# Kernel optimization log

Measured on AMD Instinct MI355X. Metric: run time of the kernel, lower is better.

Reference implementation:

```python
import jax, jax.numpy as jnp
import numpy as np
import math

D, H, FF = 1024, 16, 4096
B, L = 4, 1024

def setup_inputs() -> dict:
    key = jax.random.key(0)
    ks = jax.random.split(key, 20)
    g = lambda k, shp: jax.random.normal(k, shp, dtype=jnp.float32) * 0.02
    inp = {
        'x': jax.random.normal(ks[0], (B, L, D), dtype=jnp.float32),
        'encoder_output': jax.random.normal(ks[1], (B, L, D), dtype=jnp.float32),
        'src_mask': jnp.ones((1, 1, L, L), dtype=jnp.int32),
        'tgt_mask': jnp.tril(jnp.ones((L, L), dtype=jnp.int32))[None, None],
        'wq': g(ks[2], (D, D)), 'bq': jnp.zeros((D,), jnp.float32),
        'wk': g(ks[3], (D, D)), 'bk': jnp.zeros((D,), jnp.float32),
        'wv': g(ks[4], (D, D)), 'bv': jnp.zeros((D,), jnp.float32),
        'wo': g(ks[5], (D, D)), 'bo': jnp.zeros((D,), jnp.float32),
        'w1': g(ks[6], (FF, D)), 'b1': jnp.zeros((FF,), jnp.float32),
        'w2': g(ks[7], (D, FF)), 'b2': jnp.zeros((D,), jnp.float32),
        'g1': jnp.ones((D,), jnp.float32), 'be1': jnp.zeros((D,), jnp.float32),
        'g2': jnp.ones((D,), jnp.float32), 'be2': jnp.zeros((D,), jnp.float32),
    }
    return inp

def _layernorm(x, g, b, eps=1e-5):
    mu = jnp.mean(x, axis=-1, keepdims=True)
    var = jnp.var(x, axis=-1, keepdims=True)
    return (x - mu) * jax.lax.rsqrt(var + eps) * g + b

def _mha(q, k, v, mask, wq, bq, wk, bk, wv, bv, wo, bo):
    Bq, Lq, C = q.shape
    dh = C // H
    qh = (q @ wq.T + bq).reshape(Bq, Lq, H, dh)      # b q h d
    kh = (k @ wk.T + bk).reshape(Bq, -1, H, dh)       # b k h d
    vh = (v @ wv.T + bv).reshape(Bq, -1, H, dh)
    # NOTE: source scales by sqrt(C) (full model dim), not sqrt(head_dim)
    scores = jnp.einsum('bqhd,bkhd->bhqk', qh, kh) / math.sqrt(C)
    if mask is not None:
        scores = jnp.where(mask == 0, jnp.float32(-1e9), scores)
    attn = jax.nn.softmax(scores, axis=-1)
    out = jnp.einsum('bhqk,bkhd->bqhd', attn, vh).reshape(Bq, Lq, C)
    return out @ wo.T + bo

def reference(x, encoder_output, src_mask, tgt_mask,
              wq, bq, wk, bk, wv, bv, wo, bo,
              w1, b1, w2, b2, g1, be1, g2, be2):
    # self-attention (dropout identity in eval mode)
    y1 = _mha(x, x, x, tgt_mask, wq, bq, wk, bk, wv, bv, wo, bo)
    y1 = _layernorm(y1 + x, g1, be1)
    # cross-attention: source reuses attn1 weights and layer_norm1 (faithful)
    y2 = _mha(y1, encoder_output, encoder_output, src_mask, wq, bq, wk, bk, wv, bv, wo, bo)
    y2 = _layernorm(y1 + y2, g1, be1)
    # FFN + layer_norm2
    y = jax.nn.relu(y2 @ w1.T + b1) @ w2.T + b2
    return _layernorm(y2 + y, g2, be2)
```

## Files before the change

### kernel.cpp

```cpp
#include <hip/hip_runtime.h>
#include <hip/hip_bf16.h>

typedef __attribute__((ext_vector_type(8))) short short8;
typedef __attribute__((ext_vector_type(4))) float f32x4;
typedef __attribute__((ext_vector_type(4))) unsigned short ushort4v;

#define MFMA_BF16(a, b, c) __builtin_amdgcn_mfma_f32_16x16x32_bf16((a), (b), (c), 0, 0, 0)
#define AS1 __attribute__((address_space(1)))
#define AS3 __attribute__((address_space(3)))

__device__ __forceinline__ unsigned short f2b(float f) {
  unsigned u = __float_as_uint(f);
  u += 0x7fffu + ((u >> 16) & 1u);
  return (unsigned short)(u >> 16);
}

__device__ __forceinline__ size_t kpack_idx(int row, int col) {
  int b = row >> 10, l = row & 1023, h = col >> 6, d = col & 63;
  return ((size_t)(b * 16 + h) << 16) + l * 64 + (d ^ ((l & 7) << 3));
}

__global__ __launch_bounds__(256) void cast8(
    const float* s0, const float* s1, const float* s2, const float* s3,
    const float* s4, const float* s5, const float* s6, const float* s7,
    unsigned short* d0, unsigned short* d1, unsigned short* d2, unsigned short* d3,
    unsigned short* d4, unsigned short* d5, unsigned short* d6, unsigned short* d7,
    int n0, int n1, int n2, int n3, int n4, int n5, int n6, int n7) {
  const float* s; unsigned short* d; int n;
  switch (blockIdx.y) {
    case 0: s = s0; d = d0; n = n0; break;
    case 1: s = s1; d = d1; n = n1; break;
    case 2: s = s2; d = d2; n = n2; break;
    case 3: s = s3; d = d3; n = n3; break;
    case 4: s = s4; d = d4; n = n4; break;
    case 5: s = s5; d = d5; n = n5; break;
    case 6: s = s6; d = d6; n = n6; break;
    default: s = s7; d = d7; n = n7; break;
  }
  int stride = gridDim.x * blockDim.x;
  for (int i = blockIdx.x * blockDim.x + threadIdx.x; i < n; i += stride) {
    float4 v = reinterpret_cast<const float4*>(s)[i];
    ushort4v o;
    o.x = f2b(v.x); o.y = f2b(v.y); o.z = f2b(v.z); o.w = f2b(v.w);
    reinterpret_cast<ushort4v*>(d)[i] = o;
  }
}

template <int RELU, int RES, int OUTF, int OUTB, int TM>
__global__ __launch_bounds__(256, 4) void gemm_bt(
    const unsigned short* __restrict__ A, const unsigned short* __restrict__ W,
    const float* __restrict__ bias, const float* __restrict__ resid,
    float* __restrict__ outF, unsigned short* __restrict__ outB,
    int M, int N, int K) {
  constexpr int MI = TM / 32;
  __shared__ unsigned short lA[2][TM * 32];
  __shared__ unsigned short lB[2][128 * 32];
  int nbn = N >> 7;
  int nwg = gridDim.x;
  int id = blockIdx.x;
  { int q = nwg >> 3; id = (id & 7) * q + (id >> 3); }
  int m0 = (id / nbn) * TM, n0 = (id % nbn) << 7;
  int lane = threadIdx.x & 63, wave = threadIdx.x >> 6;
  int wr = (wave >> 1) * (TM / 2), wc = (wave & 1) * 64;
  int rq = lane & 15, kq = (lane >> 4) * 8;
  f32x4 acc[MI][4] = {};

  int e0 = threadIdx.x * 8;
#define STAGE_BT(KT, BUF)                                                       \
  {                                                                             \
    _Pragma("unroll") for (int i = 0; i < TM / 64; ++i) {                       \
      int e = e0 + i * 2048;                                                    \
      int row = e >> 5, col = e & 31;                                           \
      __builtin_amdgcn_global_load_lds(                                         \
          (const AS1 void*)(A + (size_t)(m0 + row) * K + (KT) + col),           \
          (AS3 void*)(&lA[BUF][e]), 16, 0, 0);                                  \
    }                                                                           \
    _Pragma("unroll") for (int i = 0; i < 2; ++i) {                             \
      int e = e0 + i * 2048;                                                    \
      int row = e >> 5, col = e & 31;                                           \
      __builtin_amdgcn_global_load_lds(                                         \
          (const AS1 void*)(W + (size_t)(n0 + row) * K + (KT) + col),           \
          (AS3 void*)(&lB[BUF][e]), 16, 0, 0);                                  \
    }                                                                           \
  }

  STAGE_BT(0, 0);
  __syncthreads();
  int nk = K >> 5;
  for (int t = 0; t < nk; ++t) {
    int cur = t & 1;
    if (t + 1 < nk) STAGE_BT((t + 1) << 5, cur ^ 1);
    short8 af[MI], bf[4];
#pragma unroll
    for (int i = 0; i < MI; ++i)
      af[i] = *reinterpret_cast<const short8*>(&lA[cur][(wr + i * 16 + rq) * 32 + kq]);
#pragma unroll
    for (int j = 0; j < 4; ++j)
      bf[j] = *reinterpret_cast<const short8*>(&lB[cur][(wc + j * 16 + rq) * 32 + kq]);
#pragma unroll
    for (int i = 0; i < MI; ++i)
#pragma unroll
      for (int j = 0; j < 4; ++j)
        acc[i][j] = MFMA_BF16(af[i], bf[j], acc[i][j]);
    __syncthreads();
  }
#undef STAGE_BT

  int r0 = (lane >> 4) * 4;
#pragma unroll
  for (int i = 0; i < MI; ++i) {
#pragma unroll
    for (int j = 0; j < 4; ++j) {
      int row = m0 + wr + i * 16 + r0;
      int col = n0 + wc + j * 16 + rq;
      float bv = bias[col];
#pragma unroll
      for (int r = 0; r < 4; ++r) {
        float v = acc[i][j][r] + bv;
        if (RES) v += resid[(size_t)(row + r) * N + col];
        if (RELU) v = fmaxf(v, 0.0f);
        if (OUTF) outF[(size_t)(row + r) * N + col] = v;
        if (OUTB) outB[(size_t)(row + r) * N + col] = f2b(v);
      }
    }
  }
}

__global__ __launch_bounds__(256, 4) void gemm_qkv(
    const unsigned short* __restrict__ xb, const unsigned short* __restrict__ encb,
    const unsigned short* __restrict__ wq, const unsigned short* __restrict__ wk,
    const unsigned short* __restrict__ wv,
    const float* __restrict__ bq, const float* __restrict__ bk, const float* __restrict__ bv,
    unsigned short* __restrict__ qb, unsigned short* __restrict__ kp1,
    unsigned short* __restrict__ vp1, unsigned short* __restrict__ kp2,
    unsigned short* __restrict__ vp2) {
  __shared__ unsigned short lA[2][128 * 32];
  __shared__ unsigned short lB[2][128 * 32];
  int id = blockIdx.x;
  id = (id & 7) * 160 + (id >> 3);
  int im = id / 40, jn = id % 40;
  int sel = jn >> 3;
  int m0 = im << 7, col0 = (jn & 7) << 7;
  const unsigned short* A = (sel < 3) ? xb : encb;
  const unsigned short* Wm = (sel == 0) ? wq : ((sel == 1 || sel == 3) ? wk : wv);
  const float* bias = (sel == 0) ? bq : ((sel == 1 || sel == 3) ? bk : bv);
  int lane = threadIdx.x & 63, wave = threadIdx.x >> 6;
  int wr = (wave >> 1) * 64, wc = (wave & 1) * 64;
  int rq = lane & 15, kq = (lane >> 4) * 8;
  f32x4 acc[4][4] = {};

  int e0 = threadIdx.x * 8;
#define STAGE_QKV(KT, BUF)                                                      \
  {                                                                             \
    _Pragma("unroll") for (int i = 0; i < 2; ++i) {                             \
      int e = e0 + i * 2048;                                                    \
      int row = e >> 5, col = e & 31;                                           \
      __builtin_amdgcn_global_load_lds(                                         \
          (const AS1 void*)(A + (size_t)(m0 + row) * 1024 + (KT) + col),        \
          (AS3 void*)(&lA[BUF][e]), 16, 0, 0);                                  \
      __builtin_amdgcn_global_load_lds(                                         \
          (const AS1 void*)(Wm + (size_t)(col0 + row) * 1024 + (KT) + col),     \
          (AS3 void*)(&lB[BUF][e]), 16, 0, 0);                                  \
    }                                                                           \
  }

  STAGE_QKV(0, 0);
  __syncthreads();
  for (int t = 0; t < 32; ++t) {
    int cur = t & 1;
    if (t + 1 < 32) STAGE_QKV((t + 1) << 5, cur ^ 1);
    short8 af[4], bf[4];
#pragma unroll
    for (int i = 0; i < 4; ++i)
      af[i] = *reinterpret_cast<const short8*>(&lA[cur][(wr + i * 16 + rq) * 32 + kq]);
#pragma unroll
    for (int j = 0; j < 4; ++j)
      bf[j] = *reinterpret_cast<const short8*>(&lB[cur][(wc + j * 16 + rq) * 32 + kq]);
#pragma unroll
    for (int i = 0; i < 4; ++i)
#pragma unroll
      for (int j = 0; j < 4; ++j)
        acc[i][j] = MFMA_BF16(af[i], bf[j], acc[i][j]);
    __syncthreads();
  }
#undef STAGE_QKV

  unsigned short* outp = (sel == 0) ? qb : (sel == 1) ? kp1 : (sel == 2) ? vp1
                         : (sel == 3) ? kp2 : vp2;
  int pack = (sel == 0) ? 0 : ((sel == 1 || sel == 3) ? 1 : 2);
  int r0 = (lane >> 4) * 4;
#pragma unroll
  for (int i = 0; i < 4; ++i) {
#pragma unroll
    for (int j = 0; j < 4; ++j) {
      int row0 = m0 + wr + i * 16 + r0;
      int col = col0 + wc + j * 16 + rq;
      float bv = bias[col];
      if (pack == 2) {
        int b = row0 >> 10, k0 = row0 & 1023, h = col >> 6, d = col & 63;
        size_t idx = ((size_t)((b * 16 + h) * 16 + (k0 >> 6)) << 12) + d * 64 + ((k0 & 63) ^ ((d & 7) << 3));
        ushort4v o;
        o.x = f2b(acc[i][j][0] + bv);
        o.y = f2b(acc[i][j][1] + bv);
        o.z = f2b(acc[i][j][2] + bv);
        o.w = f2b(acc[i][j][3] + bv);
        *reinterpret_cast<ushort4v*>(&outp[idx]) = o;
      } else {
#pragma unroll
        for (int r = 0; r < 4; ++r) {
          int row = row0 + r;
          float v = acc[i][j][r] + bv;
          if (pack == 0) outp[(size_t)row * 1024 + col] = f2b(v);
          else outp[kpack_idx(row, col)] = f2b(v);
        }
      }
    }
  }
}

__device__ __forceinline__ void attn_step(
    const unsigned short* __restrict__ kcur, const unsigned short* __restrict__ vcur,
    unsigned short* __restrict__ plw, const short8* qf,
    f32x4* accd, float& m2, float& lsum,
    int rq, int hi, int kq, int xr, int wave, bool domask) {
  const float SC = 0.04508422f;
  f32x4 st[4];
  __builtin_amdgcn_s_setprio(1);
#pragma unroll
  for (int sub = 0; sub < 4; ++sub) {
    f32x4 z = {0.f, 0.f, 0.f, 0.f};
#pragma unroll
    for (int c = 0; c < 2; ++c) {
      short8 kf = *reinterpret_cast<const short8*>(
          &kcur[(sub * 16 + rq) * 64 + ((c * 32 + hi * 8) ^ xr)]);
      z = MFMA_BF16(kf, qf[c], z);
    }
    st[sub] = z * SC;
  }
  __builtin_amdgcn_s_setprio(0);
  if (domask) {
#pragma unroll
    for (int sub = 0; sub < 4; ++sub)
#pragma unroll
      for (int r = 0; r < 4; ++r)
        if (sub * 16 + hi * 4 + r > wave * 16 + rq) st[sub][r] = -1e9f;
  }
  f32x4 t0 = {fmaxf(st[0][0], st[1][0]), fmaxf(st[0][1], st[1][1]),
              fmaxf(st[0][2], st[1][2]), fmaxf(st[0][3], st[1][3])};
  f32x4 t1 = {fmaxf(st[2][0], st[3][0]), fmaxf(st[2][1], st[3][1]),
              fmaxf(st[2][2], st[3][2]), fmaxf(st[2][3], st[3][3])};
  float mx = fmaxf(fmaxf(fmaxf(t0[0], t1[0]), fmaxf(t0[1], t1[1])),
                   fmaxf(fmaxf(t0[2], t1[2]), fmaxf(t0[3], t1[3])));
  mx = fmaxf(mx, __shfl_xor(mx, 16, 64));
  mx = fmaxf(mx, __shfl_xor(mx, 32, 64));
  float mn = fmaxf(m2, mx);
  float al = exp2f(m2 - mn);
  m2 = mn;
  f32x4 e[4];
#pragma unroll
  for (int sub = 0; sub < 4; ++sub)
#pragma unroll
    for (int r = 0; r < 4; ++r) e[sub][r] = exp2f(st[sub][r] - mn);
  f32x4 s01 = e[0] + e[1], s23 = e[2] + e[3];
  f32x4 s = s01 + s23;
  float ps = (s[0] + s[1]) + (s[2] + s[3]);
  ps += __shfl_xor(ps, 16, 64);
  ps += __shfl_xor(ps, 32, 64);
  lsum = lsum * al + ps;
#pragma unroll
  for (int sub = 0; sub < 4; ++sub) {
    unsigned w0 = (unsigned)f2b(e[sub][0]) | ((unsigned)f2b(e[sub][1]) << 16);
    unsigned w1 = (unsigned)f2b(e[sub][2]) | ((unsigned)f2b(e[sub][3]) << 16);
    uint2 w = make_uint2(w0, w1);
    *reinterpret_cast<uint2*>(&plw[rq * 64 + ((sub * 16 + hi * 4) ^ xr)]) = w;
  }
  float alb[4];
#pragma unroll
  for (int r = 0; r < 4; ++r) alb[r] = __shfl(al, hi * 4 + r, 64);
#pragma unroll
  for (int d = 0; d < 4; ++d)
#pragma unroll
    for (int r = 0; r < 4; ++r) accd[d][r] *= alb[r];
  short8 pf[2];
#pragma unroll
  for (int c = 0; c < 2; ++c)
    pf[c] = *reinterpret_cast<const short8*>(&plw[rq * 64 + ((c * 32 + hi * 8) ^ xr)]);
  __builtin_amdgcn_s_setprio(1);
#pragma unroll
  for (int d = 0; d < 4; ++d) {
#pragma unroll
    for (int c = 0; c < 2; ++c) {
      short8 vf = *reinterpret_cast<const short8*>(
          &vcur[(d * 16 + rq) * 64 + ((c * 32 + hi * 8) ^ xr)]);
      accd[d] = MFMA_BF16(pf[c], vf, accd[d]);
    }
  }
  __builtin_amdgcn_s_setprio(0);
}

__global__ __launch_bounds__(256) void attn_kernel(
    const unsigned short* __restrict__ Q, const unsigned short* __restrict__ Kp,
    const unsigned short* __restrict__ Vp, unsigned short* __restrict__ O, int causal) {
  __shared__ unsigned short kls[2][4096];
  __shared__ unsigned short vls[2][4096];
  __shared__ unsigned short pls[4][1024];
  int id = blockIdx.x;
  int xcd = id & 7, j = id >> 3;
  int bh = xcd * 8 + (j & 7);
  int b = bh >> 4, h = bh & 15;
  int lane = threadIdx.x & 63, wave = threadIdx.x >> 6;
  int rq = lane & 15, hi = lane >> 4, kq = hi * 8;
  int xr = (rq & 7) << 3;
  int sb = wave * 1024 + lane * 8;
  const unsigned short* Kbh = Kp + ((size_t)bh << 16);
  const unsigned short* Vbh = Vp + ((size_t)bh << 16);
  unsigned short* plw = pls[wave];

  int p = j >> 3;
  int qtA = p;
  int qtB = causal ? (15 - p) : (p + 8);
  int lastA = causal ? qtA : 15;
  int nkt = causal ? (qtB + 1) : 16;

  int qrowA = qtA * 64 + wave * 16, qrowB = qtB * 64 + wave * 16;
  short8 qfA[2], qfB[2];
#pragma unroll
  for (int c = 0; c < 2; ++c) {
    qfA[c] = *reinterpret_cast<const short8*>(
        Q + (size_t)(b * 1024 + qrowA + rq) * 1024 + h * 64 + c * 32 + kq);
    qfB[c] = *reinterpret_cast<const short8*>(
        Q + (size_t)(b * 1024 + qrowB + rq) * 1024 + h * 64 + c * 32 + kq);
  }

  float mA = -1e30f, lsA = 0.f, mB = -1e30f, lsB = 0.f;
  f32x4 accA[4] = {}, accB[4] = {};

#pragma unroll
  for (int i = 0; i < 2; ++i) {
    __builtin_amdgcn_global_load_lds((const AS1 void*)(Kbh + sb + i * 512),
                                     (AS3 void*)(&kls[0][sb + i * 512]), 16, 0, 0);
    __builtin_amdgcn_global_load_lds((const AS1 void*)(Vbh + sb + i * 512),
                                     (AS3 void*)(&vls[0][sb + i * 512]), 16, 0, 0);
  }
  __syncthreads();

  int cur = 0;
  for (int kt = 0; kt < nkt; ++kt) {
    if (kt + 1 < nkt) {
      const unsigned short* kg = Kbh + (kt + 1) * 4096 + sb;
      const unsigned short* vg = Vbh + (kt + 1) * 4096 + sb;
#pragma unroll
      for (int i = 0; i < 2; ++i) {
        __builtin_amdgcn_global_load_lds((const AS1 void*)(kg + i * 512),
                                         (AS3 void*)(&kls[cur ^ 1][sb + i * 512]), 16, 0, 0);
        __builtin_amdgcn_global_load_lds((const AS1 void*)(vg + i * 512),
                                         (AS3 void*)(&vls[cur ^ 1][sb + i * 512]), 16, 0, 0);
      }
    }
    attn_step(kls[cur], vls[cur], plw, qfB, accB, mB, lsB, rq, hi, kq, xr, wave,
              causal && kt == qtB);
    if (kt <= lastA)
      attn_step(kls[cur], vls[cur], plw, qfA, accA, mA, lsA, rq, hi, kq, xr, wave,
                causal && kt == qtA);
    __syncthreads();
    cur ^= 1;
  }

  float lbA[4], lbB[4];
#pragma unroll
  for (int r = 0; r < 4; ++r) {
    lbA[r] = 1.0f / __shfl(lsA, hi * 4 + r, 64);
    lbB[r] = 1.0f / __shfl(lsB, hi * 4 + r, 64);
  }
#pragma unroll
  for (int d = 0; d < 4; ++d)
#pragma unroll
    for (int r = 0; r < 4; ++r) {
      O[(size_t)(b * 1024 + qrowA + hi * 4 + r) * 1024 + h * 64 + d * 16 + rq] =
          f2b(accA[d][r] * lbA[r]);
      O[(size_t)(b * 1024 + qrowB + hi * 4 + r) * 1024 + h * 64 + d * 16 + rq] =
          f2b(accB[d][r] * lbB[r]);
    }
}

template <int OUTF, int OUTB>
__global__ __launch_bounds__(256) void ln_kernel(const float* __restrict__ X,
                                                 const float* __restrict__ g,
                                                 const float* __restrict__ be,
                                                 float* __restrict__ outF,
                                                 unsigned short* __restrict__ outB) {
  __shared__ float red[2][4];
  int row = blockIdx.x;
  int t = threadIdx.x;
  const float* xr = X + (size_t)row * 1024;
  float4 v = reinterpret_cast<const float4*>(xr)[t];
  float s = v.x + v.y + v.z + v.w;
  float ss = v.x * v.x + v.y * v.y + v.z * v.z + v.w * v.w;
#pragma unroll
  for (int off = 1; off < 64; off <<= 1) {
    s += __shfl_xor(s, off, 64);
    ss += __shfl_xor(ss, off, 64);
  }
  int wave = t >> 6;
  if ((t & 63) == 0) { red[0][wave] = s; red[1][wave] = ss; }
  __syncthreads();
  s = red[0][0] + red[0][1] + red[0][2] + red[0][3];
  ss = red[1][0] + red[1][1] + red[1][2] + red[1][3];
  float mu = s * (1.f / 1024.f);
  float var = ss * (1.f / 1024.f) - mu * mu;
  float rs = rsqrtf(var + 1e-5f);
  float4 gv = reinterpret_cast<const float4*>(g)[t];
  float4 bv = reinterpret_cast<const float4*>(be)[t];
  float o0 = (v.x - mu) * rs * gv.x + bv.x;
  float o1 = (v.y - mu) * rs * gv.y + bv.y;
  float o2 = (v.z - mu) * rs * gv.z + bv.z;
  float o3 = (v.w - mu) * rs * gv.w + bv.w;
  if (OUTF) {
    float4 o = make_float4(o0, o1, o2, o3);
    reinterpret_cast<float4*>(outF + (size_t)row * 1024)[t] = o;
  }
  if (OUTB) {
    ushort4v o;
    o.x = f2b(o0); o.y = f2b(o1); o.z = f2b(o2); o.w = f2b(o3);
    reinterpret_cast<ushort4v*>(outB + (size_t)row * 1024)[t] = o;
  }
}

extern "C" void kernel_launch(void* const* d_in, const int* in_sizes, int n_in,
                              void* d_out, int out_size, void* d_ws, size_t ws_size,
                              hipStream_t stream) {
  const float* x   = (const float*)d_in[0];
  const float* enc = (const float*)d_in[1];
  const float* wq = (const float*)d_in[4];  const float* bq = (const float*)d_in[5];
  const float* wk = (const float*)d_in[6];  const float* bk = (const float*)d_in[7];
  const float* wv = (const float*)d_in[8];  const float* bv = (const float*)d_in[9];
  const float* wo = (const float*)d_in[10]; const float* bo = (const float*)d_in[11];
  const float* w1 = (const float*)d_in[12]; const float* b1 = (const float*)d_in[13];
  const float* w2 = (const float*)d_in[14]; const float* b2 = (const float*)d_in[15];
  const float* g1 = (const float*)d_in[16]; const float* be1 = (const float*)d_in[17];
  const float* g2 = (const float*)d_in[18]; const float* be2 = (const float*)d_in[19];
  float* out = (float*)d_out;

  const int M = 4096;
  char* ws = (char*)d_ws;
  size_t off = 0;
  auto alloc = [&](size_t bytes) -> char* {
    char* p = ws + off;
    off += (bytes + 255) & ~(size_t)255;
    return p;
  };
  unsigned short* xb   = (unsigned short*)alloc((size_t)M * 1024 * 2);
  unsigned short* encb = (unsigned short*)alloc((size_t)M * 1024 * 2);
  unsigned short* wqb  = (unsigned short*)alloc((size_t)1024 * 1024 * 2);
  unsigned short* wkb  = (unsigned short*)alloc((size_t)1024 * 1024 * 2);
  unsigned short* wvb  = (unsigned short*)alloc((size_t)1024 * 1024 * 2);
  unsigned short* wob  = (unsigned short*)alloc((size_t)1024 * 1024 * 2);
  unsigned short* w1b  = (unsigned short*)alloc((size_t)4096 * 1024 * 2);
  unsigned short* w2b  = (unsigned short*)alloc((size_t)4096 * 1024 * 2);
  unsigned short* qb   = (unsigned short*)alloc((size_t)M * 1024 * 2);
  unsigned short* kp1  = (unsigned short*)alloc((size_t)M * 1024 * 2);
  unsigned short* vp1  = (unsigned short*)alloc((size_t)M * 1024 * 2);
  unsigned short* kp2  = (unsigned short*)alloc((size_t)M * 1024 * 2);
  unsigned short* vp2  = (unsigned short*)alloc((size_t)M * 1024 * 2);
  unsigned short* ab   = (unsigned short*)alloc((size_t)M * 1024 * 2);
  float* s1 = (float*)alloc((size_t)M * 1024 * 4);
  float* y1 = (float*)alloc((size_t)M * 1024 * 4);
  unsigned short* hb = kp1;
  unsigned short* y1b = xb;
  unsigned short* y2b = qb;
  float* y2 = y1;

  dim3 b256(256);
  cast8<<<dim3(256, 8), b256, 0, stream>>>(
      x, enc, wq, wk, wv, wo, w1, w2,
      xb, encb, wqb, wkb, wvb, wob, w1b, w2b,
      M * 1024 / 4, M * 1024 / 4, 262144, 262144, 262144, 262144,
      4096 * 1024 / 4, 4096 * 1024 / 4);

  gemm_qkv<<<1280, b256, 0, stream>>>(xb, encb, wqb, wkb, wvb, bq, bk, bv,
                                      qb, kp1, vp1, kp2, vp2);

  attn_kernel<<<512, b256, 0, stream>>>(qb, kp1, vp1, ab, 1);
  gemm_bt<0, 1, 1, 0, 64><<<512, b256, 0, stream>>>(ab, wob, bo, x, s1, nullptr, M, 1024, 1024);
  ln_kernel<1, 1><<<4096, b256, 0, stream>>>(s1, g1, be1, y1, y1b);

  gemm_bt<0, 0, 0, 1, 64><<<512, b256, 0, stream>>>(y1b, wqb, bq, nullptr, nullptr, qb, M, 1024, 1024);
  attn_kernel<<<512, b256, 0, stream>>>(qb, kp2, vp2, ab, 0);
  gemm_bt<0, 1, 1, 0, 64><<<512, b256, 0, stream>>>(ab, wob, bo, y1, s1, nullptr, M, 1024, 1024);
  ln_kernel<1, 1><<<4096, b256, 0, stream>>>(s1, g1, be1, y2, y2b);

  gemm_bt<1, 0, 0, 1, 128><<<1024, b256, 0, stream>>>(y2b, w1b, b1, nullptr, nullptr, hb, M, 4096, 1024);
  gemm_bt<0, 1, 1, 0, 64><<<512, b256, 0, stream>>>(hb, w2b, b2, y2, s1, nullptr, M, 1024, 4096);
  ln_kernel<1, 0><<<4096, b256, 0, stream>>>(s1, g2, be2, out, nullptr);

  (void)in_sizes; (void)n_in; (void)out_size; (void)ws_size;
}
```

Measured before the change: 362.3 us.

## Triple-buffer GEMM LDS staging with vmcnt waits and single barrier per k-step

Converts the double-buffered global-to-LDS staging in the generic and QKV GEMMs to a three-stage ring buffer that prefetches two k-tiles ahead. Each iteration waits only on the oldest loads with an explicit partial vmcnt and uses a single barrier instead of two. This hides more global-load latency behind MFMA work. The cost is 50% more LDS per block, which may reduce occupancy at launch_bounds(256,4), and the wait counts must exactly match the number of issued loads.

```diff
diff --git a/kernel.cpp b/kernel.cpp
--- a/kernel.cpp
+++ b/kernel.cpp
@@ -18,6 +18,15 @@
 __device__ __forceinline__ size_t kpack_idx(int row, int col) {
   int b = row >> 10, l = row & 1023, h = col >> 6, d = col & 63;
   return ((size_t)(b * 16 + h) << 16) + l * 64 + (d ^ ((l & 7) << 3));
+}
+
+template <int N>
+__device__ __forceinline__ void wait_vm() {
+  if constexpr (N == 0) asm volatile("s_waitcnt vmcnt(0)" ::: "memory");
+  else if constexpr (N == 3) asm volatile("s_waitcnt vmcnt(3)" ::: "memory");
+  else if constexpr (N == 4) asm volatile("s_waitcnt vmcnt(4)" ::: "memory");
+  else static_assert(N == 0 || N == 3 || N == 4, "unsupported vmcnt");
+  __builtin_amdgcn_sched_barrier(0);
 }
 
 __global__ __launch_bounds__(256) void cast8(
@@ -53,8 +62,9 @@
     float* __restrict__ outF, unsigned short* __restrict__ outB,
     int M, int N, int K) {
   constexpr int MI = TM / 32;
-  __shared__ unsigned short lA[2][TM * 32];
-  __shared__ unsigned short lB[2][128 * 32];
+  constexpr int NLOADS = TM / 64 + 2;
+  __shared__ unsigned short lA[3][TM * 32];
+  __shared__ unsigned short lB[3][128 * 32];
   int nbn = N >> 7;
   int nwg = gridDim.x;
   int id = blockIdx.x;
@@ -84,12 +94,15 @@
     }                                                                           \
   }
 
+  int nk = K >> 5;
   STAGE_BT(0, 0);
-  __syncthreads();
-  int nk = K >> 5;
+  STAGE_BT(32, 1);
   for (int t = 0; t < nk; ++t) {
-    int cur = t & 1;
-    if (t + 1 < nk) STAGE_BT((t + 1) << 5, cur ^ 1);
+    int cur = t % 3;
+    if (t + 1 < nk) wait_vm<NLOADS>(); else wait_vm<0>();
+    __builtin_amdgcn_s_barrier();
+    __builtin_amdgcn_sched_barrier(0);
+    if (t + 2 < nk) { int nb = (t + 2) % 3; STAGE_BT((t + 2) << 5, nb); }
     short8 af[MI], bf[4];
 #pragma unroll
     for (int i = 0; i < MI; ++i)
@@ -102,7 +115,7 @@
 #pragma unroll
       for (int j = 0; j < 4; ++j)
         acc[i][j] = MFMA_BF16(af[i], bf[j], acc[i][j]);
-    __syncthreads();
+    asm volatile("" ::: "memory");
   }
 #undef STAGE_BT
 
@@ -134,8 +147,8 @@
     unsigned short* __restrict__ qb, unsigned short* __restrict__ kp1,
     unsigned short* __restrict__ vp1, unsigned short* __restrict__ kp2,
     unsigned short* __restrict__ vp2) {
-  __shared__ unsigned short lA[2][128 * 32];
-  __shared__ unsigned short lB[2][128 * 32];
+  __shared__ unsigned short lA[3][128 * 32];
+  __shared__ unsigned short lB[3][128 * 32];
   int id = blockIdx.x;
   id = (id & 7) * 160 + (id >> 3);
   int im = id / 40, jn = id % 40;
@@ -165,10 +178,13 @@
   }
 
   STAGE_QKV(0, 0);
-  __syncthreads();
+  STAGE_QKV(32, 1);
   for (int t = 0; t < 32; ++t) {
-    int cur = t & 1;
-    if (t + 1 < 32) STAGE_QKV((t + 1) << 5, cur ^ 1);
+    int cur = t % 3;
+    if (t + 1 < 32) wait_vm<4>(); else wait_vm<0>();
+    __builtin_amdgcn_s_barrier();
+    __builtin_amdgcn_sched_barrier(0);
+    if (t + 2 < 32) { int nb = (t + 2) % 3; STAGE_QKV((t + 2) << 5, nb); }
     short8 af[4], bf[4];
 #pragma unroll
     for (int i = 0; i < 4; ++i)
@@ -181,7 +197,7 @@
 #pragma unroll
       for (int j = 0; j < 4; ++j)
         acc[i][j] = MFMA_BF16(af[i], bf[j], acc[i][j]);
-    __syncthreads();
+    asm volatile("" ::: "memory");
   }
 #undef STAGE_QKV
 
```

After: 384.2 us. +6.0%, slower.

## Add dedicated 256x256-tile FFN1 GEMM kernel with async LDS double buffering

Applied to the files above, without the earlier changes.

Replaces the generic gemm_bt launch for the first FFN projection (M=4096, N=4096, K=1024, ReLU) with a specialized kernel. It uses 512-thread blocks computing 256x256 output tiles, loads directly from global memory into LDS with global_load_lds, and double-buffers split half-K stages with explicit vmcnt waits. The larger tile is meant to raise data reuse per block and to overlap loads with MFMA work. In exchange it uses 128 KB of LDS and 128 accumulator registers per thread, and launches only 256 blocks, which may leave occupancy and load balance poor across the CUs.

```diff
diff --git a/kernel.cpp b/kernel.cpp
--- a/kernel.cpp
+++ b/kernel.cpp
@@ -18,6 +18,12 @@
 __device__ __forceinline__ size_t kpack_idx(int row, int col) {
   int b = row >> 10, l = row & 1023, h = col >> 6, d = col & 63;
   return ((size_t)(b * 16 + h) << 16) + l * 64 + (d ^ ((l & 7) << 3));
+}
+
+template <int N>
+__device__ __forceinline__ void wait_vm() {
+  if constexpr (N == 0) asm volatile("s_waitcnt vmcnt(0)" ::: "memory");
+  else asm volatile("s_waitcnt vmcnt(4)" ::: "memory");
 }
 
 __global__ __launch_bounds__(256) void cast8(
@@ -213,6 +219,99 @@
           if (pack == 0) outp[(size_t)row * 1024 + col] = f2b(v);
           else outp[kpack_idx(row, col)] = f2b(v);
         }
+      }
+    }
+  }
+}
+
+__global__ __launch_bounds__(512, 2) void ffn1_256(
+    const unsigned short* __restrict__ A, const unsigned short* __restrict__ W,
+    const float* __restrict__ bias, unsigned short* __restrict__ outB) {
+  const int K = 1024, N = 4096;
+  __shared__ unsigned short lA[2][2][8192];
+  __shared__ unsigned short lB[2][2][8192];
+  int id = blockIdx.x;
+  id = (id & 7) * 32 + (id >> 3);
+  int m0 = (id >> 4) << 8, n0 = (id & 15) << 8;
+  int tid = threadIdx.x;
+  int lane = tid & 63;
+  int wid = tid >> 6;
+  int wr = (wid >> 2) * 128, wc = (wid & 3) * 64;
+  int rq = lane & 15, hi = lane >> 4;
+  int slotx = (rq >> 1) & 3;
+  f32x4 acc[8][4] = {};
+
+#define STAGE_U(OPSEL, H, T, D)                                                 \
+  {                                                                             \
+    const unsigned short* src_ = (OPSEL) ? W : A;                               \
+    int base_ = (OPSEL) ? n0 : m0;                                              \
+    unsigned short* dst_ = (OPSEL) ? lB[D][H] : lA[D][H];                       \
+    _Pragma("unroll") for (int l = 0; l < 2; ++l) {                             \
+      int e = tid * 8 + l * 4096;                                               \
+      int row_ = e >> 5, c8 = (e >> 3) & 3;                                     \
+      int gcol = (T) * 64 + (H) * 32 + ((c8 ^ ((row_ >> 1) & 3)) << 3);         \
+      __builtin_amdgcn_global_load_lds(                                         \
+          (const AS1 void*)(src_ + (size_t)(base_ + row_) * K + gcol),          \
+          (AS3 void*)(dst_ + e), 16, 0, 0);                                     \
+    }                                                                           \
+  }
+
+  const int nk = K >> 6;
+  STAGE_U(0, 0, 0, 0); STAGE_U(1, 0, 0, 0);
+  STAGE_U(0, 1, 0, 0); STAGE_U(1, 1, 0, 0);
+  for (int t = 0; t < nk; ++t) {
+    int cur = t & 1;
+#pragma unroll
+    for (int p = 0; p < 4; ++p) {
+      constexpr int DUMMY = 0; (void)DUMMY;
+      int s = p >> 1, mh = p & 1;
+      if ((p & 1) == 0) {
+        if (t + 1 < nk) wait_vm<4>(); else wait_vm<0>();
+      }
+      __builtin_amdgcn_s_barrier();
+      if (t + 1 < nk) {
+        if (p == 0)      STAGE_U(0, 0, t + 1, cur ^ 1)
+        else if (p == 1) STAGE_U(1, 0, t + 1, cur ^ 1)
+        else if (p == 2) STAGE_U(0, 1, t + 1, cur ^ 1)
+        else             STAGE_U(1, 1, t + 1, cur ^ 1)
+      }
+      short8 af[4], bf[4];
+#pragma unroll
+      for (int i = 0; i < 4; ++i) {
+        int r = wr + (mh * 4 + i) * 16 + rq;
+        af[i] = *reinterpret_cast<const short8*>(
+            &lA[cur][s][r * 32 + ((hi ^ slotx) << 3)]);
+      }
+#pragma unroll
+      for (int j = 0; j < 4; ++j) {
+        int r = wc + j * 16 + rq;
+        bf[j] = *reinterpret_cast<const short8*>(
+            &lB[cur][s][r * 32 + ((hi ^ slotx) << 3)]);
+      }
+      __builtin_amdgcn_s_setprio(1);
+#pragma unroll
+      for (int i = 0; i < 4; ++i)
+#pragma unroll
+        for (int j = 0; j < 4; ++j)
+          acc[mh * 4 + i][j] = MFMA_BF16(af[i], bf[j], acc[mh * 4 + i][j]);
+      __builtin_amdgcn_s_setprio(0);
+      __builtin_amdgcn_s_barrier();
+    }
+  }
+#undef STAGE_U
+
+  int r0 = (lane >> 4) * 4;
+#pragma unroll
+  for (int mf = 0; mf < 8; ++mf) {
+#pragma unroll
+    for (int j = 0; j < 4; ++j) {
+      int row = m0 + wr + mf * 16 + r0;
+      int col = n0 + wc + j * 16 + rq;
+      float bv = bias[col];
+#pragma unroll
+      for (int r = 0; r < 4; ++r) {
+        float v = fmaxf(acc[mf][j][r] + bv, 0.0f);
+        outB[(size_t)(row + r) * N + col] = f2b(v);
       }
     }
   }
@@ -489,7 +588,7 @@
   gemm_bt<0, 1, 1, 0, 64><<<512, b256, 0, stream>>>(ab, wob, bo, y1, s1, nullptr, M, 1024, 1024);
   ln_kernel<1, 1><<<4096, b256, 0, stream>>>(s1, g1, be1, y2, y2b);
 
-  gemm_bt<1, 0, 0, 1, 128><<<1024, b256, 0, stream>>>(y2b, w1b, b1, nullptr, nullptr, hb, M, 4096, 1024);
+  ffn1_256<<<256, dim3(512), 0, stream>>>(y2b, w1b, b1, hb);
   gemm_bt<0, 1, 1, 0, 64><<<512, b256, 0, stream>>>(hb, w2b, b2, y2, s1, nullptr, M, 1024, 4096);
   ln_kernel<1, 0><<<4096, b256, 0, stream>>>(s1, g2, be2, out, nullptr);
 
```

Result: no change. 364.6 us (+0.6%).
